# Kernel optimization log

Hardware: AMD Instinct MI355X
Metric: run time of the kernel (lower is better)

Reference implementation:

```python
import jax, jax.numpy as jnp
import numpy as np

B, S, D = 4, 2048, 1024
H = 16
HD = D // H  # 64


def setup_inputs() -> dict:
    key = jax.random.key(0)
    ks = jax.random.split(key, 5)
    s = 0.02
    return {
        "x": jax.random.normal(ks[0], (B, S, D), dtype=jnp.float32),
        "w_qkv": jax.random.normal(ks[1], (D, 3 * D), dtype=jnp.float32) * s,
        "b_qkv": jnp.zeros((3 * D,), dtype=jnp.float32),
        "w_out": jax.random.normal(ks[2], (D, D), dtype=jnp.float32) * s,
        "b_out": jnp.zeros((D,), dtype=jnp.float32),
    }


def reference(x, w_qkv, b_qkv, w_out, b_out):
    b, s, d = x.shape
    qkv = x @ w_qkv + b_qkv                              # [b,s,3d]
    qkv = qkv.reshape(b, s, 3, H, HD)
    q = qkv[:, :, 0].transpose(0, 2, 1, 3)               # [b,h,s,hd]
    k = qkv[:, :, 1].transpose(0, 2, 1, 3)
    v = qkv[:, :, 2].transpose(0, 2, 1, 3)
    scale = 1.0 / jnp.sqrt(jnp.asarray(HD, dtype=x.dtype))
    scores = jnp.einsum("bhqd,bhkd->bhqk", q, k) * scale  # [b,h,s,s]
    causal = jnp.tril(jnp.ones((s, s), dtype=bool))
    scores = jnp.where(causal[None, None], scores, jnp.asarray(-jnp.inf, dtype=x.dtype))
    probs = jax.nn.softmax(scores, axis=-1)
    out = jnp.einsum("bhqk,bhkd->bhqd", probs, v)        # [b,h,s,hd]
    out = out.transpose(0, 2, 1, 3).reshape(b, s, d)
    return out @ w_out + b_out
```

## Files before the change

### kernel.cpp

```cpp
#include <hip/hip_runtime.h>
#include <hip/hip_bf16.h>

typedef __bf16 bf16_t;
typedef __bf16 bf16x4 __attribute__((ext_vector_type(4)));
typedef __bf16 bf16x8 __attribute__((ext_vector_type(8)));
typedef float f32x4 __attribute__((ext_vector_type(4)));

#define Bb 4
#define Ss 2048
#define Dd 1024
#define Hh 16
#define HDd 64

#define QSC 0.1803368801111244f

__device__ __forceinline__ void gld16(const bf16_t* g, bf16_t* l) {
  __builtin_amdgcn_global_load_lds(
      (const __attribute__((address_space(1))) unsigned int*)g,
      (__attribute__((address_space(3))) unsigned int*)l, 16, 0, 0);
}

__global__ __launch_bounds__(256) void conv_to_bf16(
    const float* __restrict__ src, bf16_t* __restrict__ dst) {
  int i = (blockIdx.x * 256 + threadIdx.x) * 4;
  float4 v = *(const float4*)&src[i];
  bf16x4 o = {(bf16_t)v.x, (bf16_t)v.y, (bf16_t)v.z, (bf16_t)v.w};
  *(bf16x4*)&dst[i] = o;
}

__global__ __launch_bounds__(256) void transpose_conv(
    const float* __restrict__ in, bf16_t* __restrict__ out, int R, int C) {
  __shared__ bf16_t tile[32][33];
  int c0 = blockIdx.x * 32, r0 = blockIdx.y * 32;
  int tx = threadIdx.x, ty = threadIdx.y;
#pragma unroll
  for (int j = 0; j < 32; j += 8)
    tile[ty + j][tx] = (bf16_t)in[(size_t)(r0 + ty + j) * C + c0 + tx];
  __syncthreads();
#pragma unroll
  for (int j = 0; j < 32; j += 8)
    out[(size_t)(c0 + ty + j) * R + r0 + tx] = tile[tx][ty + j];
}

template <int MODE>
__global__ __launch_bounds__(256, 2) void gemm_ring(
    const bf16_t* __restrict__ A, const bf16_t* __restrict__ Bt,
    const float* __restrict__ bias, float* __restrict__ outf,
    bf16_t* __restrict__ out0, bf16_t* __restrict__ out1,
    bf16_t* __restrict__ out2, int M, int N, int K) {
  const int tid = threadIdx.x;
  const int lane = tid & 63;
  const int wave = tid >> 6;
  const int quad = lane >> 4;
  const int lr = lane & 15;
  const int wr = wave >> 1;
  const int wc = wave & 1;
  const int m0 = blockIdx.y * 256;
  const int n0 = blockIdx.x * 128;

  __shared__ __align__(16) bf16_t As[3][256 * 32];
  __shared__ __align__(16) bf16_t Bs[3][128 * 32];

  const f32x4 zero = {0.f, 0.f, 0.f, 0.f};
  f32x4 acc[8][4];
#pragma unroll
  for (int mi = 0; mi < 8; ++mi)
#pragma unroll
    for (int ni = 0; ni < 4; ++ni) acc[mi][ni] = zero;

  int ar[4], ac[4], br[2], bc[2];
#pragma unroll
  for (int i = 0; i < 4; ++i) {
    int c = tid + i * 256;
    ar[i] = c >> 2;
    ac[i] = ((c & 3) ^ ((ar[i] >> 1) & 3)) * 8;
  }
#pragma unroll
  for (int i = 0; i < 2; ++i) {
    int c = tid + i * 256;
    br[i] = c >> 2;
    bc[i] = ((c & 3) ^ ((br[i] >> 1) & 3)) * 8;
  }

  const int nk = K >> 5;

  auto stage = [&](int t, int s) {
    const int ko = t << 5;
#pragma unroll
    for (int i = 0; i < 4; ++i)
      gld16(&A[(size_t)(m0 + ar[i]) * K + ko + ac[i]],
            &As[s][(tid + i * 256) * 8]);
#pragma unroll
    for (int i = 0; i < 2; ++i)
      gld16(&Bt[(size_t)(n0 + br[i]) * K + ko + bc[i]],
            &Bs[s][(tid + i * 256) * 8]);
  };

  stage(0, 0);
  if (nk > 1) {
    stage(1, 1);
    asm volatile("s_waitcnt vmcnt(6)" ::: "memory");
  } else {
    asm volatile("s_waitcnt vmcnt(0)" ::: "memory");
  }
  __builtin_amdgcn_s_barrier();

  const int qx = (quad ^ ((lr >> 1) & 3)) * 8;

  int scur = 0;
  for (int t = 0; t < nk; ++t) {
    const bool more2 = (t + 2 < nk);
    if (more2) {
      int s2 = scur + 2;
      if (s2 >= 3) s2 -= 3;
      stage(t + 2, s2);
    }
    bf16x8 af[8], bfr[4];
#pragma unroll
    for (int mi = 0; mi < 8; ++mi)
      af[mi] = *(const bf16x8*)&As[scur][(wr * 128 + mi * 16 + lr) * 32 + qx];
#pragma unroll
    for (int ni = 0; ni < 4; ++ni)
      bfr[ni] = *(const bf16x8*)&Bs[scur][(wc * 64 + ni * 16 + lr) * 32 + qx];
    __builtin_amdgcn_s_setprio(1);
#pragma unroll
    for (int mi = 0; mi < 8; ++mi)
#pragma unroll
      for (int ni = 0; ni < 4; ++ni)
        acc[mi][ni] = __builtin_amdgcn_mfma_f32_16x16x32_bf16(
            af[mi], bfr[ni], acc[mi][ni], 0, 0, 0);
    __builtin_amdgcn_s_setprio(0);
    if (t + 1 < nk) {
      if (more2)
        asm volatile("s_waitcnt vmcnt(6)" ::: "memory");
      else
        asm volatile("s_waitcnt vmcnt(0)" ::: "memory");
      __builtin_amdgcn_s_barrier();
    }
    scur = (scur == 2) ? 0 : scur + 1;
  }

#pragma unroll
  for (int mi = 0; mi < 8; ++mi) {
    const int mbase = m0 + wr * 128 + mi * 16 + quad * 4;
#pragma unroll
    for (int ni = 0; ni < 4; ++ni) {
      const int n = n0 + wc * 64 + ni * 16 + lr;
      const float bv = bias[n];
      if (MODE == 1) {
#pragma unroll
        for (int r = 0; r < 4; ++r)
          outf[(size_t)(mbase + r) * N + n] = acc[mi][ni][r] + bv;
      } else {
        const int which = n >> 10;
        const int h = (n >> 6) & 15;
        const int hd = n & 63;
        const int b = mbase >> 11;
        const int s = mbase & 2047;
        if (which == 2) {
          bf16x4 pk = {(bf16_t)(acc[mi][ni][0] + bv),
                       (bf16_t)(acc[mi][ni][1] + bv),
                       (bf16_t)(acc[mi][ni][2] + bv),
                       (bf16_t)(acc[mi][ni][3] + bv)};
          *(bf16x4*)&out2[(((size_t)(b * Hh + h)) * HDd + hd) * Ss + s] = pk;
        } else {
          bf16_t* dst = (which == 0) ? out0 : out1;
          const float sc = (which == 0) ? QSC : 1.0f;
#pragma unroll
          for (int r = 0; r < 4; ++r)
            dst[(((size_t)(b * Hh + h)) * Ss + s + r) * HDd + hd] =
                (bf16_t)((acc[mi][ni][r] + bv) * sc);
        }
      }
    }
  }
}

__global__ __launch_bounds__(256) void attn_kernel(
    const bf16_t* __restrict__ Qg, const bf16_t* __restrict__ Kg,
    const bf16_t* __restrict__ Vtg, bf16_t* __restrict__ Og) {
  const int tid = threadIdx.x;
  const int lane = tid & 63;
  const int wave = tid >> 6;
  const int quad = lane >> 4;
  const int lr = lane & 15;

  const int bid = blockIdx.x;
  const int xcd = bid & 7;
  const int j = bid >> 3;
  const int bh = xcd * 8 + (j >> 3);
  const int p = j & 7;
  const int b = bh >> 4;
  const int h = bh & 15;
  const int wq = wave * 32;

  const bf16_t* Qp = Qg + (size_t)bh * Ss * HDd;
  const bf16_t* Kp = Kg + (size_t)bh * Ss * HDd;
  const bf16_t* Vp = Vtg + (size_t)bh * HDd * Ss;

  __shared__ bf16_t Ks[2][64 * 72];
  __shared__ bf16_t Vts[2][64 * 72];
  __shared__ bf16_t Ps[4][32 * 72];

  bf16x8 kreg[2], vreg[2];
  const int r0 = tid >> 3;
  const int c0 = (tid & 7) * 8;

  const f32x4 zero = {0.f, 0.f, 0.f, 0.f};

#pragma unroll
  for (int i = 0; i < 2; ++i) {
    kreg[i] = *(const bf16x8*)&Kp[(size_t)(r0 + i * 32) * HDd + c0];
    vreg[i] = *(const bf16x8*)&Vp[(size_t)(r0 + i * 32) * Ss + c0];
  }

  int cur = 0;
  for (int half = 0; half < 2; ++half) {
    const int qt = half ? p : 15 - p;
    const int qbase = qt * 128;
    const int ktiles = qt * 2 + 2;

    bf16x8 bq[2][2];
#pragma unroll
    for (int qt2 = 0; qt2 < 2; ++qt2)
#pragma unroll
      for (int kk2 = 0; kk2 < 2; ++kk2)
        bq[qt2][kk2] = *(const bf16x8*)&Qp[(size_t)(qbase + wq + qt2 * 16 +
                                                    lr) *
                                               HDd +
                                           kk2 * 32 + quad * 8];

    f32x4 oacc[4][2];
#pragma unroll
    for (int dt = 0; dt < 4; ++dt)
#pragma unroll
      for (int qt2 = 0; qt2 < 2; ++qt2) oacc[dt][qt2] = zero;
    float l_run[2] = {0.f, 0.f};

    for (int kt = 0; kt < ktiles; ++kt) {
      const int kbase = kt * 64;

#pragma unroll
      for (int i = 0; i < 2; ++i) {
        *(bf16x8*)&Ks[cur][(r0 + i * 32) * 72 + c0] = kreg[i];
        *(bf16x8*)&Vts[cur][(r0 + i * 32) * 72 + c0] = vreg[i];
      }
      __syncthreads();

      const int nkb = (kt + 1 < ktiles) ? kbase + 64 : 0;
#pragma unroll
      for (int i = 0; i < 2; ++i) {
        kreg[i] = *(const bf16x8*)&Kp[(size_t)(nkb + r0 + i * 32) * HDd + c0];
        vreg[i] = *(const bf16x8*)&Vp[(size_t)(r0 + i * 32) * Ss + nkb + c0];
      }

      f32x4 sacc[4][2];
#pragma unroll
      for (int kt4 = 0; kt4 < 4; ++kt4)
#pragma unroll
        for (int qt2 = 0; qt2 < 2; ++qt2) sacc[kt4][qt2] = zero;
#pragma unroll
      for (int kk2 = 0; kk2 < 2; ++kk2) {
        bf16x8 ak[4];
#pragma unroll
        for (int kt4 = 0; kt4 < 4; ++kt4)
          ak[kt4] = *(const bf16x8*)&Ks[cur][(kt4 * 16 + lr) * 72 + kk2 * 32 +
                                             quad * 8];
#pragma unroll
        for (int kt4 = 0; kt4 < 4; ++kt4)
#pragma unroll
          for (int qt2 = 0; qt2 < 2; ++qt2)
            sacc[kt4][qt2] = __builtin_amdgcn_mfma_f32_16x16x32_bf16(
                ak[kt4], bq[qt2][kk2], sacc[kt4][qt2], 0, 0, 0);
      }

      const bool edge = (kt >= 2 * qt);
#pragma unroll
      for (int kt4 = 0; kt4 < 4; ++kt4)
#pragma unroll
        for (int qt2 = 0; qt2 < 2; ++qt2)
#pragma unroll
          for (int r = 0; r < 4; ++r) {
            float s = sacc[kt4][qt2][r];
            if (edge) {
              const int qg = qbase + wq + qt2 * 16 + lr;
              const int kg = kbase + kt4 * 16 + quad * 4 + r;
              if (kg > qg) s = -1e30f;
            }
            const float pv = __builtin_amdgcn_exp2f(s);
            sacc[kt4][qt2][r] = pv;
            l_run[qt2] += pv;
          }

#pragma unroll
      for (int kt4 = 0; kt4 < 4; ++kt4)
#pragma unroll
        for (int qt2 = 0; qt2 < 2; ++qt2) {
          bf16x4 pk = {(bf16_t)sacc[kt4][qt2][0], (bf16_t)sacc[kt4][qt2][1],
                       (bf16_t)sacc[kt4][qt2][2], (bf16_t)sacc[kt4][qt2][3]};
          *(bf16x4*)&Ps[wave][(qt2 * 16 + lr) * 72 + kt4 * 16 + quad * 4] = pk;
        }

#pragma unroll
      for (int kk2 = 0; kk2 < 2; ++kk2) {
        bf16x8 av[4], bp[2];
#pragma unroll
        for (int dt = 0; dt < 4; ++dt)
          av[dt] = *(const bf16x8*)&Vts[cur][(dt * 16 + lr) * 72 + kk2 * 32 +
                                             quad * 8];
#pragma unroll
        for (int qt2 = 0; qt2 < 2; ++qt2)
          bp[qt2] = *(const bf16x8*)&Ps[wave][(qt2 * 16 + lr) * 72 + kk2 * 32 +
                                              quad * 8];
#pragma unroll
        for (int dt = 0; dt < 4; ++dt)
#pragma unroll
          for (int qt2 = 0; qt2 < 2; ++qt2)
            oacc[dt][qt2] = __builtin_amdgcn_mfma_f32_16x16x32_bf16(
                av[dt], bp[qt2], oacc[dt][qt2], 0, 0, 0);
      }
      cur ^= 1;
    }

#pragma unroll
    for (int qt2 = 0; qt2 < 2; ++qt2) {
      l_run[qt2] += __shfl_xor(l_run[qt2], 16, 64);
      l_run[qt2] += __shfl_xor(l_run[qt2], 32, 64);
    }

#pragma unroll
    for (int qt2 = 0; qt2 < 2; ++qt2) {
      const float inv = 1.f / l_run[qt2];
      const int qg = qbase + wq + qt2 * 16 + lr;
#pragma unroll
      for (int dt = 0; dt < 4; ++dt) {
        bf16x4 ov = {(bf16_t)(oacc[dt][qt2][0] * inv),
                     (bf16_t)(oacc[dt][qt2][1] * inv),
                     (bf16_t)(oacc[dt][qt2][2] * inv),
                     (bf16_t)(oacc[dt][qt2][3] * inv)};
        *(bf16x4*)&Og[((size_t)b * Ss + qg) * Dd + h * HDd + dt * 16 +
                      quad * 4] = ov;
      }
    }
  }
}

extern "C" void kernel_launch(void* const* d_in, const int* in_sizes, int n_in,
                              void* d_out, int out_size, void* d_ws,
                              size_t ws_size, hipStream_t stream) {
  const float* x = (const float*)d_in[0];
  const float* w_qkv = (const float*)d_in[1];
  const float* b_qkv = (const float*)d_in[2];
  const float* w_out = (const float*)d_in[3];
  const float* b_out = (const float*)d_in[4];
  float* out = (float*)d_out;

  bf16_t* Kb = (bf16_t*)d_ws;
  bf16_t* Vt = Kb + (size_t)Bb * Hh * Ss * HDd;
  bf16_t* slot3 = Vt + (size_t)Bb * Hh * Ss * HDd;
  bf16_t* Wt1 = slot3;
  bf16_t* Ob = slot3;
  bf16_t* Wt2 = Kb;
  bf16_t* Qb = (bf16_t*)d_out;
  bf16_t* Xc = (bf16_t*)d_out + (size_t)8192 * 1024;

  conv_to_bf16<<<8192, 256, 0, stream>>>(x, Xc);
  transpose_conv<<<dim3(96, 32), dim3(32, 8), 0, stream>>>(w_qkv, Wt1, 1024,
                                                           3072);

  gemm_ring<0><<<dim3(24, 32), 256, 0, stream>>>(
      Xc, Wt1, b_qkv, nullptr, Qb, Kb, Vt, 8192, 3072, 1024);

  attn_kernel<<<dim3(512), 256, 0, stream>>>(Qb, Kb, Vt, Ob);

  transpose_conv<<<dim3(32, 32), dim3(32, 8), 0, stream>>>(w_out, Wt2, 1024,
                                                           1024);

  gemm_ring<1><<<dim3(8, 32), 256, 0, stream>>>(
      Ob, Wt2, b_out, out, nullptr, nullptr, nullptr, 8192, 1024, 1024);
}
```

Measured before the change: 288.3 us.

## Restructure GEMM to 8 waves with 64-wide K tiles and split staging

The bf16 GEMM used for the QKV and output projections now runs with 512 threads (8 waves), each wave owning a 64x64 output tile instead of 128x64. The K tile grows from 32 to 64 with a new XOR swizzle, and each K step is split into two MFMA sub-steps. The A and B global-to-LDS prefetches are issued separately, one in each sub-step, with extra barriers. The goal is better latency hiding and fewer loop iterations, at the cost of about 147KB of LDS per block, which limits occupancy to one block per CU.

```diff
diff --git a/kernel.cpp b/kernel.cpp
--- a/kernel.cpp
+++ b/kernel.cpp
@@ -43,7 +43,7 @@
 }
 
 template <int MODE>
-__global__ __launch_bounds__(256, 2) void gemm_ring(
+__global__ __launch_bounds__(512, 2) void gemm_8p(
     const bf16_t* __restrict__ A, const bf16_t* __restrict__ Bt,
     const float* __restrict__ bias, float* __restrict__ outf,
     bf16_t* __restrict__ out0, bf16_t* __restrict__ out1,
@@ -58,91 +58,105 @@
   const int m0 = blockIdx.y * 256;
   const int n0 = blockIdx.x * 128;
 
-  __shared__ __align__(16) bf16_t As[3][256 * 32];
-  __shared__ __align__(16) bf16_t Bs[3][128 * 32];
+  __shared__ __align__(16) bf16_t As[3][256 * 64];
+  __shared__ __align__(16) bf16_t Bs[3][128 * 64];
 
   const f32x4 zero = {0.f, 0.f, 0.f, 0.f};
-  f32x4 acc[8][4];
-#pragma unroll
-  for (int mi = 0; mi < 8; ++mi)
+  f32x4 acc[4][4];
+#pragma unroll
+  for (int mi = 0; mi < 4; ++mi)
 #pragma unroll
     for (int ni = 0; ni < 4; ++ni) acc[mi][ni] = zero;
 
   int ar[4], ac[4], br[2], bc[2];
 #pragma unroll
   for (int i = 0; i < 4; ++i) {
-    int c = tid + i * 256;
-    ar[i] = c >> 2;
-    ac[i] = ((c & 3) ^ ((ar[i] >> 1) & 3)) * 8;
+    int c = tid + i * 512;
+    ar[i] = c >> 3;
+    ac[i] = ((c & 7) ^ (ar[i] & 7)) * 8;
   }
 #pragma unroll
   for (int i = 0; i < 2; ++i) {
-    int c = tid + i * 256;
-    br[i] = c >> 2;
-    bc[i] = ((c & 3) ^ ((br[i] >> 1) & 3)) * 8;
-  }
-
-  const int nk = K >> 5;
-
-  auto stage = [&](int t, int s) {
-    const int ko = t << 5;
+    int c = tid + i * 512;
+    br[i] = c >> 3;
+    bc[i] = ((c & 7) ^ (br[i] & 7)) * 8;
+  }
+
+  const int nk = K >> 6;
+
+  auto stageA = [&](int t, int s) {
+    const int ko = t << 6;
 #pragma unroll
     for (int i = 0; i < 4; ++i)
       gld16(&A[(size_t)(m0 + ar[i]) * K + ko + ac[i]],
-            &As[s][(tid + i * 256) * 8]);
+            &As[s][(tid + i * 512) * 8]);
+  };
+  auto stageB = [&](int t, int s) {
+    const int ko = t << 6;
 #pragma unroll
     for (int i = 0; i < 2; ++i)
       gld16(&Bt[(size_t)(n0 + br[i]) * K + ko + bc[i]],
-            &Bs[s][(tid + i * 256) * 8]);
+            &Bs[s][(tid + i * 512) * 8]);
   };
 
-  stage(0, 0);
-  if (nk > 1) {
-    stage(1, 1);
-    asm volatile("s_waitcnt vmcnt(6)" ::: "memory");
-  } else {
-    asm volatile("s_waitcnt vmcnt(0)" ::: "memory");
-  }
+  stageA(0, 0); stageB(0, 0);
+  stageA(1, 1); stageB(1, 1);
+  asm volatile("s_waitcnt vmcnt(6)" ::: "memory");
   __builtin_amdgcn_s_barrier();
 
-  const int qx = (quad ^ ((lr >> 1) & 3)) * 8;
+  const int sx = lr & 7;
+  const int arow = wr * 64 + lr;
+  const int brow = wc * 64 + lr;
 
   int scur = 0;
   for (int t = 0; t < nk; ++t) {
-    const bool more2 = (t + 2 < nk);
-    if (more2) {
-      int s2 = scur + 2;
-      if (s2 >= 3) s2 -= 3;
-      stage(t + 2, s2);
-    }
-    bf16x8 af[8], bfr[4];
-#pragma unroll
-    for (int mi = 0; mi < 8; ++mi)
-      af[mi] = *(const bf16x8*)&As[scur][(wr * 128 + mi * 16 + lr) * 32 + qx];
-#pragma unroll
-    for (int ni = 0; ni < 4; ++ni)
-      bfr[ni] = *(const bf16x8*)&Bs[scur][(wc * 64 + ni * 16 + lr) * 32 + qx];
-    __builtin_amdgcn_s_setprio(1);
-#pragma unroll
-    for (int mi = 0; mi < 8; ++mi)
+    const bf16_t* as = As[scur];
+    const bf16_t* bs = Bs[scur];
+    int s2 = scur + 2;
+    if (s2 >= 3) s2 -= 3;
+    const bool pre = (t + 2 < nk);
+#pragma unroll
+    for (int ks = 0; ks < 2; ++ks) {
+      bf16x8 af[4], bfr[4];
+      const int cx = (((ks << 2) | quad) ^ sx) * 8;
+#pragma unroll
+      for (int mi = 0; mi < 4; ++mi)
+        af[mi] = *(const bf16x8*)&as[(arow + mi * 16) * 64 + cx];
 #pragma unroll
       for (int ni = 0; ni < 4; ++ni)
-        acc[mi][ni] = __builtin_amdgcn_mfma_f32_16x16x32_bf16(
-            af[mi], bfr[ni], acc[mi][ni], 0, 0, 0);
-    __builtin_amdgcn_s_setprio(0);
-    if (t + 1 < nk) {
-      if (more2)
-        asm volatile("s_waitcnt vmcnt(6)" ::: "memory");
-      else
-        asm volatile("s_waitcnt vmcnt(0)" ::: "memory");
+        bfr[ni] = *(const bf16x8*)&bs[(brow + ni * 16) * 64 + cx];
+      if (ks == 0) {
+        if (pre) stageA(t + 2, s2);
+      } else {
+        if (pre) stageB(t + 2, s2);
+      }
       __builtin_amdgcn_s_barrier();
+      asm volatile("s_waitcnt lgkmcnt(0)" ::: "memory");
+      __builtin_amdgcn_sched_barrier(0);
+      __builtin_amdgcn_s_setprio(1);
+#pragma unroll
+      for (int mi = 0; mi < 4; ++mi)
+#pragma unroll
+        for (int ni = 0; ni < 4; ++ni)
+          acc[mi][ni] = __builtin_amdgcn_mfma_f32_16x16x32_bf16(
+              af[mi], bfr[ni], acc[mi][ni], 0, 0, 0);
+      __builtin_amdgcn_s_setprio(0);
+      if (ks == 0) {
+        __builtin_amdgcn_s_barrier();
+      } else if (t + 1 < nk) {
+        if (pre)
+          asm volatile("s_waitcnt vmcnt(6)" ::: "memory");
+        else
+          asm volatile("s_waitcnt vmcnt(0)" ::: "memory");
+        __builtin_amdgcn_s_barrier();
+      }
     }
     scur = (scur == 2) ? 0 : scur + 1;
   }
 
 #pragma unroll
-  for (int mi = 0; mi < 8; ++mi) {
-    const int mbase = m0 + wr * 128 + mi * 16 + quad * 4;
+  for (int mi = 0; mi < 4; ++mi) {
+    const int mbase = m0 + wr * 64 + mi * 16 + quad * 4;
 #pragma unroll
     for (int ni = 0; ni < 4; ++ni) {
       const int n = n0 + wc * 64 + ni * 16 + lr;
@@ -368,7 +382,7 @@
   transpose_conv<<<dim3(96, 32), dim3(32, 8), 0, stream>>>(w_qkv, Wt1, 1024,
                                                            3072);
 
-  gemm_ring<0><<<dim3(24, 32), 256, 0, stream>>>(
+  gemm_8p<0><<<dim3(24, 32), 512, 0, stream>>>(
       Xc, Wt1, b_qkv, nullptr, Qb, Kb, Vt, 8192, 3072, 1024);
 
   attn_kernel<<<dim3(512), 256, 0, stream>>>(Qb, Kb, Vt, Ob);
@@ -376,6 +390,6 @@
   transpose_conv<<<dim3(32, 32), dim3(32, 8), 0, stream>>>(w_out, Wt2, 1024,
                                                            1024);
 
-  gemm_ring<1><<<dim3(8, 32), 256, 0, stream>>>(
+  gemm_8p<1><<<dim3(8, 32), 512, 0, stream>>>(
       Ob, Wt2, b_out, out, nullptr, nullptr, nullptr, 8192, 1024, 1024);
 }
```

Measured after the change: 262.0 us. -9.1%, faster.
